# Optimization experiments

Hardware: AMD Instinct MI355X
Metric: run time of the kernel (lower is better)

## Reference

```python
import jax, jax.numpy as jnp
import numpy as np

B, N, D, H = 4, 2048, 256, 4
DH = D // H
SS = DH ** -0.25  # sqrt(scale), applied to both qk0 and qk1
EPS = 1e-5


def _split_heads(t):
    # [B, N, D] -> [B, H, N, DH]
    b, n, _ = t.shape
    return t.reshape(b, n, H, DH).transpose(0, 2, 1, 3)


def _merge_heads(t):
    # [B, H, N, DH] -> [B, N, D]
    b, h, n, dh = t.shape
    return t.transpose(0, 2, 1, 3).reshape(b, n, h * dh)


def _layernorm(x, g, b):
    mu = jnp.mean(x, axis=-1, keepdims=True)
    var = jnp.mean(jnp.square(x - mu), axis=-1, keepdims=True)
    return (x - mu) * jax.lax.rsqrt(var + EPS) * g + b


def setup_inputs() -> dict:
    key = jax.random.key(0)
    ks = jax.random.split(key, 16)
    s = 0.02
    return {
        "x0": jax.random.normal(ks[0], (B, N, D), jnp.float32),
        "x1": jax.random.normal(ks[1], (B, N, D), jnp.float32),
        # weights stored as [in, out] (y = x @ W + b), matching torch Linear math
        "Wqk": jax.random.normal(ks[2], (D, D), jnp.float32) * s,
        "bqk": jnp.zeros((D,), jnp.float32),
        "Wv": jax.random.normal(ks[3], (D, D), jnp.float32) * s,
        "bv": jnp.zeros((D,), jnp.float32),
        "Wo": jax.random.normal(ks[4], (D, D), jnp.float32) * s,
        "bo": jnp.zeros((D,), jnp.float32),
        "W1": jax.random.normal(ks[5], (2 * D, 2 * D), jnp.float32) * s,
        "b1": jnp.zeros((2 * D,), jnp.float32),
        "ln_g": jnp.ones((2 * D,), jnp.float32),
        "ln_b": jnp.zeros((2 * D,), jnp.float32),
        "W2": jax.random.normal(ks[6], (2 * D, D), jnp.float32) * s,
        "b2": jnp.zeros((D,), jnp.float32),
    }


def reference(x0, x1, Wqk, bqk, Wv, bv, Wo, bo, W1, b1, ln_g, ln_b, W2, b2):
    qk0 = _split_heads(x0 @ Wqk + bqk) * SS  # [B,H,N,DH]
    qk1 = _split_heads(x1 @ Wqk + bqk) * SS
    v0 = _split_heads(x0 @ Wv + bv)
    v1 = _split_heads(x1 @ Wv + bv)

    # single shared similarity matrix, reused for both softmax directions
    sim = jnp.einsum("bhid,bhjd->bhij", qk0, qk1)  # [B,H,N0,N1]
    attn01 = jax.nn.softmax(sim, axis=-1)                      # rows over j
    attn10 = jax.nn.softmax(jnp.swapaxes(sim, -1, -2), axis=-1)  # rows over i

    m0 = jnp.einsum("bhij,bhjd->bhid", attn01, v1)  # [B,H,N0,DH]
    m1 = jnp.einsum("bhji,bhjd->bhid", jnp.swapaxes(attn10, -1, -2), v0)

    m0 = _merge_heads(m0) @ Wo + bo  # [B,N,D]
    m1 = _merge_heads(m1) @ Wo + bo

    def ffn(x, m):
        h = jnp.concatenate([x, m], axis=-1) @ W1 + b1
        h = jax.nn.gelu(_layernorm(h, ln_g, ln_b), approximate=False)
        return x + h @ W2 + b2

    return ffn(x0, m0), ffn(x1, m1)
```

## Files before the change

### kernel.cpp

```cpp
#include <hip/hip_runtime.h>
#include <hip/hip_bf16.h>
#include <math.h>

#define DEV static __device__ __forceinline__

typedef float f32x4 __attribute__((ext_vector_type(4)));
typedef short s16x8 __attribute__((ext_vector_type(8)));
typedef unsigned short u16;
typedef unsigned int u32;

#define ROWS 16384
#define SSCALE 0.35355339059327379f

DEV f32x4 mfma16(s16x8 a, s16x8 b, f32x4 c) {
  return __builtin_amdgcn_mfma_f32_16x16x32_bf16(a, b, c, 0, 0, 0);
}

DEV float bf2f(u16 x) { u32 u = ((u32)x) << 16; float f; __builtin_memcpy(&f, &u, 4); return f; }
DEV u16 f2bf(float x) { __hip_bfloat16 b = __float2bfloat16(x); u16 r; __builtin_memcpy(&r, &b, 2); return r; }

DEV void gload_lds16(const void* g, void* l) {
  __builtin_amdgcn_global_load_lds((const __attribute__((address_space(1))) u32*)g,
                                   (__attribute__((address_space(3))) u32*)l, 16, 0, 0);
}

__global__ __launch_bounds__(256) void k_prep(
    const float* __restrict__ x0, const float* __restrict__ x1,
    const float* __restrict__ Wqk, const float* __restrict__ Wv,
    const float* __restrict__ Wo, const float* __restrict__ W1,
    const float* __restrict__ W2,
    u16* __restrict__ bt_qkv, u16* __restrict__ bt_o,
    u16* __restrict__ bt_1, u16* __restrict__ bt_2, u16* __restrict__ Xb)
{
  int tid = blockIdx.x * 256 + threadIdx.x;
  if (tid < 131072) {
    int c = tid >> 8, k = tid & 255;
    float v = (c < 256) ? Wqk[k * 256 + c] : Wv[k * 256 + (c - 256)];
    bt_qkv[tid] = f2bf(v);
  } else if (tid < 131072 + 65536) {
    int t = tid - 131072; int c = t >> 8, k = t & 255;
    bt_o[t] = f2bf(Wo[k * 256 + c]);
  } else if (tid < 131072 + 65536 + 262144) {
    int t = tid - (131072 + 65536); int c = t >> 9, k = t & 511;
    bt_1[t] = f2bf(W1[k * 512 + c]);
  } else if (tid < 589824) {
    int t = tid - (131072 + 65536 + 262144); int c = t >> 9, k = t & 511;
    bt_2[t] = f2bf(W2[k * 256 + c]);
  } else {
    int t = tid - 589824;
    float v = (t < 8192 * 256) ? x0[t] : x1[t - 8192 * 256];
    Xb[t] = f2bf(v);
  }
}

template <int KD, int K1, int EPI>
__global__ __launch_bounds__(256, 2) void k_gemm(
    const u16* __restrict__ A1, const u16* __restrict__ A2,
    const u16* __restrict__ Bt,
    const float* __restrict__ bias, const float* __restrict__ bias2,
    const float* __restrict__ res0, const float* __restrict__ res1,
    u16* __restrict__ outb, u16* __restrict__ outb2,
    float* __restrict__ outf, int Ncols)
{
  __shared__ char lds[32768];
  char* ldsA = lds;
  char* ldsB = lds + 16384;
  const int tid = threadIdx.x;
  const int lane = tid & 63;
  const int w = tid >> 6;
  const int wm = w >> 1, wn = w & 1;
  const int g = lane >> 4, li = lane & 15;
  const int m0 = blockIdx.x * 128, n0 = blockIdx.y * 128;

  auto stage = [&](int buf, int t) {
    const int k0 = t * 32;
#pragma unroll
    for (int it = 0; it < 2; ++it) {
      int chunk = it * 256 + w * 64 + lane;
      int row = chunk >> 2, c = chunk & 3;
      int kc = k0 + ((c ^ ((row >> 1) & 3)) << 3);
      const u16* src = (kc < K1) ? (A1 + (size_t)(m0 + row) * K1 + kc)
                                 : (A2 + (size_t)(m0 + row) * (KD - K1) + (kc - K1));
      gload_lds16(src, ldsA + buf * 8192 + (it * 256 + w * 64) * 16);
    }
#pragma unroll
    for (int it = 0; it < 2; ++it) {
      int chunk = it * 256 + w * 64 + lane;
      int row = chunk >> 2, c = chunk & 3;
      int kc = k0 + ((c ^ ((row >> 1) & 3)) << 3);
      gload_lds16(Bt + (size_t)(n0 + row) * KD + kc,
                  ldsB + buf * 8192 + (it * 256 + w * 64) * 16);
    }
  };

  f32x4 acc[4][4] = {};

  stage(0, 0);
  __syncthreads();
  const int NT = KD / 32;
  for (int t = 0; t < NT; ++t) {
    if (t + 1 < NT) stage((t + 1) & 1, t + 1);
    const char* bufA = ldsA + (t & 1) * 8192;
    const char* bufB = ldsB + (t & 1) * 8192;
    s16x8 af[4], bfr[4];
#pragma unroll
    for (int rt = 0; rt < 4; ++rt) {
      int row = wm * 64 + rt * 16 + li;
      af[rt] = *(const s16x8*)(bufA + row * 64 + ((g ^ ((row >> 1) & 3)) << 4));
    }
#pragma unroll
    for (int ct = 0; ct < 4; ++ct) {
      int col = wn * 64 + ct * 16 + li;
      bfr[ct] = *(const s16x8*)(bufB + col * 64 + ((g ^ ((col >> 1) & 3)) << 4));
    }
#pragma unroll
    for (int rt = 0; rt < 4; ++rt)
#pragma unroll
      for (int ct = 0; ct < 4; ++ct)
        acc[rt][ct] = mfma16(af[rt], bfr[ct], acc[rt][ct]);
    __syncthreads();
  }

#pragma unroll
  for (int rt = 0; rt < 4; ++rt) {
#pragma unroll
    for (int ct = 0; ct < 4; ++ct) {
#pragma unroll
      for (int r = 0; r < 4; ++r) {
        int grow = m0 + wm * 64 + rt * 16 + g * 4 + r;
        int gcol = n0 + wn * 64 + ct * 16 + li;
        float v = acc[rt][ct][r];
        if (EPI == 0) {
          int dir = grow >> 13, b = (grow >> 11) & 3, n = grow & 2047;
          if (gcol < 256) {
            int h = gcol >> 6, dh = gcol & 63;
            float q = (v + bias[gcol]) * SSCALE;
            outb[((size_t)(dir * 16 + b * 4 + h) * 2048 + n) * 64 + dh] = f2bf(q);
          } else {
            int c2 = gcol - 256; int h = c2 >> 6, dh = c2 & 63;
            outb2[((size_t)(dir * 16 + b * 4 + h) * 64 + dh) * 2048 + n] = f2bf(v + bias2[c2]);
          }
        } else if (EPI == 1) {
          outb[(size_t)grow * Ncols + gcol] = f2bf(v + bias[gcol]);
        } else {
          float x = (grow < 8192) ? res0[(size_t)grow * 256 + gcol]
                                  : res1[(size_t)(grow - 8192) * 256 + gcol];
          outf[(size_t)grow * 256 + gcol] = v + bias[gcol] + x;
        }
      }
    }
  }
}

__global__ __launch_bounds__(256, 2) void k_attn(
    const u16* __restrict__ qk, const u16* __restrict__ vt, u16* __restrict__ m_all)
{
  __shared__ char Kl[2][8192];
  __shared__ char Vl[2][8192];
  __shared__ char Pl[4][4096];
  const int tid = threadIdx.x, lane = tid & 63, w = tid >> 6;
  const int g = lane >> 4, li = lane & 15;
  const int qblk = blockIdx.x & 15;
  const int p = blockIdx.x >> 4;
  const int dir = p & 1;
  const int bh = p >> 1;
  const char* Qg = (const char*)qk + ((size_t)(dir * 16 + bh)) * 2048 * 64 * 2;
  const char* Kg = (const char*)qk + ((size_t)((dir ^ 1) * 16 + bh)) * 2048 * 64 * 2;
  const char* Vg = (const char*)vt + ((size_t)((dir ^ 1) * 16 + bh)) * 64 * 2048 * 2;
  const int q0 = qblk * 128 + w * 32;

  s16x8 qf[2][2];
#pragma unroll
  for (int qt = 0; qt < 2; ++qt)
#pragma unroll
    for (int ks = 0; ks < 2; ++ks)
      qf[qt][ks] = *(const s16x8*)(Qg + (size_t)(q0 + qt * 16 + li) * 128 + ks * 64 + g * 16);

  auto stageKV = [&](int buf, int jt) {
#pragma unroll
    for (int it = 0; it < 2; ++it) {
      int chunk = it * 256 + w * 64 + lane;
      int row = chunk >> 3, c = chunk & 7;
      int cc = (c ^ (row & 7)) << 4;
      gload_lds16(Kg + (size_t)(jt * 64 + row) * 128 + cc, &Kl[buf][(it * 256 + w * 64) * 16]);
    }
#pragma unroll
    for (int it = 0; it < 2; ++it) {
      int chunk = it * 256 + w * 64 + lane;
      int row = chunk >> 3, c = chunk & 7;
      int cc = (c ^ (row & 7)) << 4;
      gload_lds16(Vg + (size_t)row * 4096 + jt * 128 + cc, &Vl[buf][(it * 256 + w * 64) * 16]);
    }
  };

  f32x4 acco[2][4] = {};
  float accl[2][4] = {};

  stageKV(0, 0);
  __syncthreads();
  for (int jt = 0; jt < 32; ++jt) {
    if (jt + 1 < 32) stageKV((jt + 1) & 1, jt + 1);
    const char* Kb = Kl[jt & 1];
    const char* Vb = Vl[jt & 1];

    s16x8 vf[4][2];
#pragma unroll
    for (int dt = 0; dt < 4; ++dt)
#pragma unroll
      for (int ks = 0; ks < 2; ++ks) {
        int row = dt * 16 + li;
        vf[dt][ks] = *(const s16x8*)(Vb + row * 128 + (((ks * 4 + g) ^ (row & 7)) << 4));
      }

#pragma unroll
    for (int qt = 0; qt < 2; ++qt) {
#pragma unroll
      for (int kt = 0; kt < 4; ++kt) {
        f32x4 s = {0.f, 0.f, 0.f, 0.f};
#pragma unroll
        for (int ks = 0; ks < 2; ++ks) {
          int row = kt * 16 + li;
          s16x8 kf = *(const s16x8*)(Kb + row * 128 + (((ks * 4 + g) ^ (row & 7)) << 4));
          s = mfma16(qf[qt][ks], kf, s);
        }
#pragma unroll
        for (int r = 0; r < 4; ++r) {
          float pv = __expf(s[r]);
          accl[qt][r] += pv;
          int q = qt * 16 + g * 4 + r;
          int key = kt * 16 + li;
          *(u16*)(&Pl[w][q * 128 + ((key * 2) ^ ((q & 7) << 4))]) = f2bf(pv);
        }
      }
    }

#pragma unroll
    for (int qt = 0; qt < 2; ++qt) {
      s16x8 pf[2];
#pragma unroll
      for (int ks = 0; ks < 2; ++ks) {
        int qrow = qt * 16 + li;
        pf[ks] = *(const s16x8*)(&Pl[w][qrow * 128 + (((ks * 4 + g) << 4) ^ ((qrow & 7) << 4))]);
      }
#pragma unroll
      for (int dt = 0; dt < 4; ++dt)
#pragma unroll
        for (int ks = 0; ks < 2; ++ks)
          acco[qt][dt] = mfma16(pf[ks], vf[dt][ks], acco[qt][dt]);
    }
    __syncthreads();
  }

  float inv[2][4];
#pragma unroll
  for (int qt = 0; qt < 2; ++qt)
#pragma unroll
    for (int r = 0; r < 4; ++r) {
      float v = accl[qt][r];
      v += __shfl_xor(v, 1); v += __shfl_xor(v, 2);
      v += __shfl_xor(v, 4); v += __shfl_xor(v, 8);
      inv[qt][r] = 1.0f / v;
    }

  const int b = bh >> 2, h = bh & 3;
  const size_t rowbase = (size_t)dir * 8192 + (size_t)b * 2048 + q0;
#pragma unroll
  for (int qt = 0; qt < 2; ++qt)
#pragma unroll
    for (int dt = 0; dt < 4; ++dt)
#pragma unroll
      for (int r = 0; r < 4; ++r) {
        int q = qt * 16 + g * 4 + r;
        int dh = dt * 16 + li;
        m_all[(rowbase + q) * 256 + h * 64 + dh] = f2bf(acco[qt][dt][r] * inv[qt][r]);
      }
}

__global__ __launch_bounds__(256) void k_ln_gelu(
    const u16* __restrict__ h, const float* __restrict__ lg,
    const float* __restrict__ lb, u16* __restrict__ o)
{
  int lane = threadIdx.x & 63;
  size_t row = blockIdx.x * 4 + (threadIdx.x >> 6);
  s16x8 v = *(const s16x8*)(h + row * 512 + lane * 8);
  float f[8], s = 0.f, s2 = 0.f;
#pragma unroll
  for (int j = 0; j < 8; ++j) { f[j] = bf2f((u16)v[j]); s += f[j]; s2 += f[j] * f[j]; }
#pragma unroll
  for (int m = 1; m < 64; m <<= 1) { s += __shfl_xor(s, m); s2 += __shfl_xor(s2, m); }
  float mu = s * (1.0f / 512.0f);
  float var = s2 * (1.0f / 512.0f) - mu * mu;
  float rs = rsqrtf(var + 1e-5f);
  s16x8 ov;
#pragma unroll
  for (int j = 0; j < 8; ++j) {
    int c = lane * 8 + j;
    float y = (f[j] - mu) * rs * lg[c] + lb[c];
    float ge = 0.5f * y * (1.0f + erff(y * 0.70710678118654752f));
    ov[j] = (short)f2bf(ge);
  }
  *(s16x8*)(o + row * 512 + lane * 8) = ov;
}

extern "C" void kernel_launch(void* const* d_in, const int* in_sizes, int n_in,
                              void* d_out, int out_size, void* d_ws, size_t ws_size,
                              hipStream_t stream)
{
  const float* x0  = (const float*)d_in[0];
  const float* x1  = (const float*)d_in[1];
  const float* Wqk = (const float*)d_in[2];
  const float* bqk = (const float*)d_in[3];
  const float* Wv  = (const float*)d_in[4];
  const float* bv  = (const float*)d_in[5];
  const float* Wo  = (const float*)d_in[6];
  const float* bo  = (const float*)d_in[7];
  const float* W1  = (const float*)d_in[8];
  const float* b1  = (const float*)d_in[9];
  const float* lg  = (const float*)d_in[10];
  const float* lb  = (const float*)d_in[11];
  const float* W2  = (const float*)d_in[12];
  const float* b2  = (const float*)d_in[13];
  float* out = (float*)d_out;
  char* ws = (char*)d_ws;

  u16* Xb    = (u16*)(ws + 0);
  u16* qk    = (u16*)(ws + 8388608);
  u16* vt    = (u16*)(ws + 16777216);
  u16* m_all = (u16*)(ws + 25165824);
  u16* mo    = (u16*)(ws + 33554432);
  u16* hpre  = (u16*)(ws + 41943040);
  u16* gact  = (u16*)(ws + 58720256);
  u16* btqkv = (u16*)(ws + 75497472);
  u16* bto   = (u16*)(ws + 75759616);
  u16* bt1   = (u16*)(ws + 75890688);
  u16* bt2   = (u16*)(ws + 76414976);

  k_prep<<<dim3(18688), dim3(256), 0, stream>>>(x0, x1, Wqk, Wv, Wo, W1, W2,
                                                btqkv, bto, bt1, bt2, Xb);
  k_gemm<256, 256, 0><<<dim3(128, 4), dim3(256), 0, stream>>>(
      Xb, nullptr, btqkv, bqk, bv, nullptr, nullptr, qk, vt, nullptr, 512);
  k_attn<<<dim3(512), dim3(256), 0, stream>>>(qk, vt, m_all);
  k_gemm<256, 256, 1><<<dim3(128, 2), dim3(256), 0, stream>>>(
      m_all, nullptr, bto, bo, nullptr, nullptr, nullptr, mo, nullptr, nullptr, 256);
  k_gemm<512, 256, 1><<<dim3(128, 4), dim3(256), 0, stream>>>(
      Xb, mo, bt1, b1, nullptr, nullptr, nullptr, hpre, nullptr, nullptr, 512);
  k_ln_gelu<<<dim3(4096), dim3(256), 0, stream>>>(hpre, lg, lb, gact);
  k_gemm<512, 512, 3><<<dim3(128, 2), dim3(256), 0, stream>>>(
      gact, nullptr, bt2, b2, nullptr, x0, x1, nullptr, nullptr, out, 256);
}
```

Before: 257.3 us.

## Split attention keys across two blocks, add combine kernel, narrow GEMM tiles

Attention now splits the key range in half, so twice as many blocks run. Each block writes unnormalized fp32 partial outputs and row sums, and a new combine kernel adds them and normalizes to bf16. The S tile is computed transposed (K as the A operand), so P can be written to LDS as packed 8-byte stores and the row sums need fewer shuffles. The Wo and W2 GEMMs get a BN=64 tile variant to double their grid, and the V-transpose epilogue uses packed 4-wide stores. This adds an extra launch and fp32 partial traffic in exchange for better occupancy on the 256-CU part.

```diff
diff --git a/kernel.cpp b/kernel.cpp
--- a/kernel.cpp
+++ b/kernel.cpp
@@ -8,6 +8,8 @@
 typedef short s16x8 __attribute__((ext_vector_type(8)));
 typedef unsigned short u16;
 typedef unsigned int u32;
+typedef u32 u32x2 __attribute__((ext_vector_type(2)));
+typedef u16 u16x4 __attribute__((ext_vector_type(4)));
 
 #define ROWS 16384
 #define SSCALE 0.35355339059327379f
@@ -53,7 +55,7 @@
   }
 }
 
-template <int KD, int K1, int EPI>
+template <int KD, int K1, int EPI, int BN>
 __global__ __launch_bounds__(256, 2) void k_gemm(
     const u16* __restrict__ A1, const u16* __restrict__ A2,
     const u16* __restrict__ Bt,
@@ -62,15 +64,17 @@
     u16* __restrict__ outb, u16* __restrict__ outb2,
     float* __restrict__ outf, int Ncols)
 {
-  __shared__ char lds[32768];
+  constexpr int MR = (BN == 128) ? 4 : 2;
+  __shared__ char lds[16384 + 2 * BN * 64];
   char* ldsA = lds;
   char* ldsB = lds + 16384;
   const int tid = threadIdx.x;
   const int lane = tid & 63;
   const int w = tid >> 6;
-  const int wm = w >> 1, wn = w & 1;
+  const int wm = (BN == 128) ? (w >> 1) : w;
+  const int wn = (BN == 128) ? (w & 1) : 0;
   const int g = lane >> 4, li = lane & 15;
-  const int m0 = blockIdx.x * 128, n0 = blockIdx.y * 128;
+  const int m0 = blockIdx.x * 128, n0 = blockIdx.y * BN;
 
   auto stage = [&](int buf, int t) {
     const int k0 = t * 32;
@@ -84,16 +88,16 @@
       gload_lds16(src, ldsA + buf * 8192 + (it * 256 + w * 64) * 16);
     }
 #pragma unroll
-    for (int it = 0; it < 2; ++it) {
+    for (int it = 0; it < BN / 64; ++it) {
       int chunk = it * 256 + w * 64 + lane;
       int row = chunk >> 2, c = chunk & 3;
       int kc = k0 + ((c ^ ((row >> 1) & 3)) << 3);
       gload_lds16(Bt + (size_t)(n0 + row) * KD + kc,
-                  ldsB + buf * 8192 + (it * 256 + w * 64) * 16);
+                  ldsB + buf * (BN * 64) + (it * 256 + w * 64) * 16);
     }
   };
 
-  f32x4 acc[4][4] = {};
+  f32x4 acc[MR][4] = {};
 
   stage(0, 0);
   __syncthreads();
@@ -101,11 +105,11 @@
   for (int t = 0; t < NT; ++t) {
     if (t + 1 < NT) stage((t + 1) & 1, t + 1);
     const char* bufA = ldsA + (t & 1) * 8192;
-    const char* bufB = ldsB + (t & 1) * 8192;
-    s16x8 af[4], bfr[4];
-#pragma unroll
-    for (int rt = 0; rt < 4; ++rt) {
-      int row = wm * 64 + rt * 16 + li;
+    const char* bufB = ldsB + (t & 1) * (BN * 64);
+    s16x8 af[MR], bfr[4];
+#pragma unroll
+    for (int rt = 0; rt < MR; ++rt) {
+      int row = wm * (MR * 16) + rt * 16 + li;
       af[rt] = *(const s16x8*)(bufA + row * 64 + ((g ^ ((row >> 1) & 3)) << 4));
     }
 #pragma unroll
@@ -114,7 +118,7 @@
       bfr[ct] = *(const s16x8*)(bufB + col * 64 + ((g ^ ((col >> 1) & 3)) << 4));
     }
 #pragma unroll
-    for (int rt = 0; rt < 4; ++rt)
+    for (int rt = 0; rt < MR; ++rt)
 #pragma unroll
       for (int ct = 0; ct < 4; ++ct)
         acc[rt][ct] = mfma16(af[rt], bfr[ct], acc[rt][ct]);
@@ -122,38 +126,47 @@
   }
 
 #pragma unroll
-  for (int rt = 0; rt < 4; ++rt) {
+  for (int rt = 0; rt < MR; ++rt) {
 #pragma unroll
     for (int ct = 0; ct < 4; ++ct) {
-#pragma unroll
-      for (int r = 0; r < 4; ++r) {
-        int grow = m0 + wm * 64 + rt * 16 + g * 4 + r;
-        int gcol = n0 + wn * 64 + ct * 16 + li;
-        float v = acc[rt][ct][r];
-        if (EPI == 0) {
-          int dir = grow >> 13, b = (grow >> 11) & 3, n = grow & 2047;
-          if (gcol < 256) {
-            int h = gcol >> 6, dh = gcol & 63;
-            float q = (v + bias[gcol]) * SSCALE;
-            outb[((size_t)(dir * 16 + b * 4 + h) * 2048 + n) * 64 + dh] = f2bf(q);
-          } else {
-            int c2 = gcol - 256; int h = c2 >> 6, dh = c2 & 63;
-            outb2[((size_t)(dir * 16 + b * 4 + h) * 64 + dh) * 2048 + n] = f2bf(v + bias2[c2]);
+      const int growb = m0 + wm * (MR * 16) + rt * 16 + g * 4;
+      const int gcol = n0 + wn * 64 + ct * 16 + li;
+      if (EPI == 0) {
+        const int dir = growb >> 13, b = (growb >> 11) & 3, n = growb & 2047;
+        if (gcol < 256) {
+          const int h = gcol >> 6, dh = gcol & 63;
+#pragma unroll
+          for (int r = 0; r < 4; ++r) {
+            float q = (acc[rt][ct][r] + bias[gcol]) * SSCALE;
+            outb[((size_t)(dir * 16 + b * 4 + h) * 2048 + (n + r)) * 64 + dh] = f2bf(q);
           }
-        } else if (EPI == 1) {
-          outb[(size_t)grow * Ncols + gcol] = f2bf(v + bias[gcol]);
         } else {
+          const int c2 = gcol - 256, h = c2 >> 6, dh = c2 & 63;
+          u16x4 pk;
+#pragma unroll
+          for (int r = 0; r < 4; ++r) pk[r] = f2bf(acc[rt][ct][r] + bias2[c2]);
+          *(u16x4*)(outb2 + ((size_t)(dir * 16 + b * 4 + h) * 64 + dh) * 2048 + n) = pk;
+        }
+      } else if (EPI == 1) {
+#pragma unroll
+        for (int r = 0; r < 4; ++r)
+          outb[(size_t)(growb + r) * Ncols + gcol] = f2bf(acc[rt][ct][r] + bias[gcol]);
+      } else {
+#pragma unroll
+        for (int r = 0; r < 4; ++r) {
+          int grow = growb + r;
           float x = (grow < 8192) ? res0[(size_t)grow * 256 + gcol]
                                   : res1[(size_t)(grow - 8192) * 256 + gcol];
-          outf[(size_t)grow * 256 + gcol] = v + bias[gcol] + x;
+          outf[(size_t)grow * 256 + gcol] = acc[rt][ct][r] + bias[gcol] + x;
         }
       }
     }
   }
 }
 
-__global__ __launch_bounds__(256, 2) void k_attn(
-    const u16* __restrict__ qk, const u16* __restrict__ vt, u16* __restrict__ m_all)
+__global__ __launch_bounds__(256, 3) void k_attn(
+    const u16* __restrict__ qk, const u16* __restrict__ vt,
+    float* __restrict__ Opart, float* __restrict__ lpart)
 {
   __shared__ char Kl[2][8192];
   __shared__ char Vl[2][8192];
@@ -161,12 +174,14 @@
   const int tid = threadIdx.x, lane = tid & 63, w = tid >> 6;
   const int g = lane >> 4, li = lane & 15;
   const int qblk = blockIdx.x & 15;
-  const int p = blockIdx.x >> 4;
+  const int half = (blockIdx.x >> 4) & 1;
+  const int p = blockIdx.x >> 5;
   const int dir = p & 1;
   const int bh = p >> 1;
-  const char* Qg = (const char*)qk + ((size_t)(dir * 16 + bh)) * 2048 * 64 * 2;
-  const char* Kg = (const char*)qk + ((size_t)((dir ^ 1) * 16 + bh)) * 2048 * 64 * 2;
-  const char* Vg = (const char*)vt + ((size_t)((dir ^ 1) * 16 + bh)) * 64 * 2048 * 2;
+  const int pidx = dir * 16 + bh;
+  const char* Qg = (const char*)qk + (size_t)pidx * 2048 * 128;
+  const char* Kg = (const char*)qk + (size_t)((dir ^ 1) * 16 + bh) * 2048 * 128;
+  const char* Vg = (const char*)vt + (size_t)((dir ^ 1) * 16 + bh) * 2048 * 128;
   const int q0 = qblk * 128 + w * 32;
 
   s16x8 qf[2][2];
@@ -177,103 +192,117 @@
       qf[qt][ks] = *(const s16x8*)(Qg + (size_t)(q0 + qt * 16 + li) * 128 + ks * 64 + g * 16);
 
   auto stageKV = [&](int buf, int jt) {
+    const size_t krow0 = (size_t)(half * 1024 + jt * 64);
 #pragma unroll
     for (int it = 0; it < 2; ++it) {
       int chunk = it * 256 + w * 64 + lane;
       int row = chunk >> 3, c = chunk & 7;
       int cc = (c ^ (row & 7)) << 4;
-      gload_lds16(Kg + (size_t)(jt * 64 + row) * 128 + cc, &Kl[buf][(it * 256 + w * 64) * 16]);
+      gload_lds16(Kg + (krow0 + row) * 128 + cc, &Kl[buf][(it * 256 + w * 64) * 16]);
     }
 #pragma unroll
     for (int it = 0; it < 2; ++it) {
       int chunk = it * 256 + w * 64 + lane;
       int row = chunk >> 3, c = chunk & 7;
       int cc = (c ^ (row & 7)) << 4;
-      gload_lds16(Vg + (size_t)row * 4096 + jt * 128 + cc, &Vl[buf][(it * 256 + w * 64) * 16]);
+      gload_lds16(Vg + (size_t)row * 4096 + half * 2048 + jt * 128 + cc,
+                  &Vl[buf][(it * 256 + w * 64) * 16]);
     }
   };
 
   f32x4 acco[2][4] = {};
-  float accl[2][4] = {};
+  float accl[2] = {0.f, 0.f};
 
   stageKV(0, 0);
   __syncthreads();
-  for (int jt = 0; jt < 32; ++jt) {
-    if (jt + 1 < 32) stageKV((jt + 1) & 1, jt + 1);
+  for (int jt = 0; jt < 16; ++jt) {
+    if (jt + 1 < 16) stageKV((jt + 1) & 1, jt + 1);
     const char* Kb = Kl[jt & 1];
     const char* Vb = Vl[jt & 1];
 
-    s16x8 vf[4][2];
-#pragma unroll
-    for (int dt = 0; dt < 4; ++dt)
-#pragma unroll
-      for (int ks = 0; ks < 2; ++ks) {
-        int row = dt * 16 + li;
-        vf[dt][ks] = *(const s16x8*)(Vb + row * 128 + (((ks * 4 + g) ^ (row & 7)) << 4));
+#pragma unroll
+    for (int kt = 0; kt < 4; ++kt) {
+      const int krow = kt * 16 + li;
+      s16x8 kf0 = *(const s16x8*)(Kb + krow * 128 + ((g ^ (krow & 7)) << 4));
+      s16x8 kf1 = *(const s16x8*)(Kb + krow * 128 + (((4 + g) ^ (krow & 7)) << 4));
+#pragma unroll
+      for (int qt = 0; qt < 2; ++qt) {
+        f32x4 s = {0.f, 0.f, 0.f, 0.f};
+        s = mfma16(kf0, qf[qt][0], s);
+        s = mfma16(kf1, qf[qt][1], s);
+        float p0 = __expf(s[0]), p1 = __expf(s[1]);
+        float p2 = __expf(s[2]), p3 = __expf(s[3]);
+        accl[qt] += (p0 + p1) + (p2 + p3);
+        u32x2 pk;
+        pk.x = (u32)f2bf(p0) | ((u32)f2bf(p1) << 16);
+        pk.y = (u32)f2bf(p2) | ((u32)f2bf(p3) << 16);
+        int addr = ((qt * 16 + li) * 128 + kt * 32 + g * 8) ^ ((li & 7) << 4);
+        *(u32x2*)(&Pl[w][addr]) = pk;
       }
-
-#pragma unroll
-    for (int qt = 0; qt < 2; ++qt) {
-#pragma unroll
-      for (int kt = 0; kt < 4; ++kt) {
-        f32x4 s = {0.f, 0.f, 0.f, 0.f};
-#pragma unroll
-        for (int ks = 0; ks < 2; ++ks) {
-          int row = kt * 16 + li;
-          s16x8 kf = *(const s16x8*)(Kb + row * 128 + (((ks * 4 + g) ^ (row & 7)) << 4));
-          s = mfma16(qf[qt][ks], kf, s);
-        }
-#pragma unroll
-        for (int r = 0; r < 4; ++r) {
-          float pv = __expf(s[r]);
-          accl[qt][r] += pv;
-          int q = qt * 16 + g * 4 + r;
-          int key = kt * 16 + li;
-          *(u16*)(&Pl[w][q * 128 + ((key * 2) ^ ((q & 7) << 4))]) = f2bf(pv);
-        }
+    }
+
+#pragma unroll
+    for (int ks = 0; ks < 2; ++ks) {
+      s16x8 vfr[4];
+#pragma unroll
+      for (int dt = 0; dt < 4; ++dt) {
+        const int vrow = dt * 16 + li;
+        vfr[dt] = *(const s16x8*)(Vb + vrow * 128 + (((ks * 4 + g) ^ (vrow & 7)) << 4));
       }
-    }
-
-#pragma unroll
-    for (int qt = 0; qt < 2; ++qt) {
-      s16x8 pf[2];
-#pragma unroll
-      for (int ks = 0; ks < 2; ++ks) {
-        int qrow = qt * 16 + li;
-        pf[ks] = *(const s16x8*)(&Pl[w][qrow * 128 + (((ks * 4 + g) << 4) ^ ((qrow & 7) << 4))]);
+#pragma unroll
+      for (int qt = 0; qt < 2; ++qt) {
+        s16x8 pf = *(const s16x8*)(
+            &Pl[w][((qt * 16 + li) * 128 + ks * 64 + g * 16) ^ ((li & 7) << 4)]);
+#pragma unroll
+        for (int dt = 0; dt < 4; ++dt)
+          acco[qt][dt] = mfma16(pf, vfr[dt], acco[qt][dt]);
       }
-#pragma unroll
-      for (int dt = 0; dt < 4; ++dt)
-#pragma unroll
-        for (int ks = 0; ks < 2; ++ks)
-          acco[qt][dt] = mfma16(pf[ks], vf[dt][ks], acco[qt][dt]);
     }
     __syncthreads();
   }
 
-  float inv[2][4];
-#pragma unroll
-  for (int qt = 0; qt < 2; ++qt)
-#pragma unroll
-    for (int r = 0; r < 4; ++r) {
-      float v = accl[qt][r];
-      v += __shfl_xor(v, 1); v += __shfl_xor(v, 2);
-      v += __shfl_xor(v, 4); v += __shfl_xor(v, 8);
-      inv[qt][r] = 1.0f / v;
-    }
+#pragma unroll
+  for (int qt = 0; qt < 2; ++qt) {
+    float v = accl[qt];
+    v += __shfl_xor(v, 16);
+    v += __shfl_xor(v, 32);
+    accl[qt] = v;
+  }
 
   const int b = bh >> 2, h = bh & 3;
   const size_t rowbase = (size_t)dir * 8192 + (size_t)b * 2048 + q0;
+  float* Oh = Opart + (size_t)half * 4194304;
 #pragma unroll
   for (int qt = 0; qt < 2; ++qt)
 #pragma unroll
     for (int dt = 0; dt < 4; ++dt)
 #pragma unroll
-      for (int r = 0; r < 4; ++r) {
-        int q = qt * 16 + g * 4 + r;
-        int dh = dt * 16 + li;
-        m_all[(rowbase + q) * 256 + h * 64 + dh] = f2bf(acco[qt][dt][r] * inv[qt][r]);
-      }
+      for (int r = 0; r < 4; ++r)
+        Oh[(rowbase + qt * 16 + g * 4 + r) * 256 + h * 64 + dt * 16 + li] = acco[qt][dt][r];
+  if (lane < 16) {
+#pragma unroll
+    for (int qt = 0; qt < 2; ++qt)
+      lpart[half * 65536 + pidx * 2048 + q0 + qt * 16 + li] = accl[qt];
+  }
+}
+
+__global__ __launch_bounds__(256) void k_combine(
+    const float* __restrict__ Op, const float* __restrict__ lp,
+    u16* __restrict__ m_all)
+{
+  int t = blockIdx.x * 256 + threadIdx.x;
+  int row = t >> 6, quad = t & 63;
+  int dh0 = quad * 4;
+  int dir = row >> 13, b = (row >> 11) & 3, n = row & 2047, h = dh0 >> 6;
+  int pidx = dir * 16 + b * 4 + h;
+  float l = lp[pidx * 2048 + n] + lp[65536 + pidx * 2048 + n];
+  float invl = 1.0f / l;
+  f32x4 o0 = *(const f32x4*)(Op + (size_t)row * 256 + dh0);
+  f32x4 o1 = *(const f32x4*)(Op + 4194304 + (size_t)row * 256 + dh0);
+  u16x4 r4;
+#pragma unroll
+  for (int j = 0; j < 4; ++j) r4[j] = f2bf((o0[j] + o1[j]) * invl);
+  *(u16x4*)(m_all + (size_t)row * 256 + dh0) = r4;
 }
 
 __global__ __launch_bounds__(256) void k_ln_gelu(
@@ -323,28 +352,31 @@
   float* out = (float*)d_out;
   char* ws = (char*)d_ws;
 
-  u16* Xb    = (u16*)(ws + 0);
-  u16* qk    = (u16*)(ws + 8388608);
-  u16* vt    = (u16*)(ws + 16777216);
-  u16* m_all = (u16*)(ws + 25165824);
-  u16* mo    = (u16*)(ws + 33554432);
-  u16* hpre  = (u16*)(ws + 41943040);
-  u16* gact  = (u16*)(ws + 58720256);
-  u16* btqkv = (u16*)(ws + 75497472);
-  u16* bto   = (u16*)(ws + 75759616);
-  u16* bt1   = (u16*)(ws + 75890688);
-  u16* bt2   = (u16*)(ws + 76414976);
+  u16*   Xb    = (u16*)(ws + 0);
+  u16*   qk    = (u16*)(ws + 8388608);
+  u16*   vt    = (u16*)(ws + 16777216);
+  u16*   m_all = (u16*)(ws + 25165824);
+  float* lpart = (float*)(ws + 33554432);
+  u16*   mo    = (u16*)(ws + 34078720);
+  float* Opart = (float*)(ws + 42467328);
+  u16*   hpre  = (u16*)(ws + 42467328);
+  u16*   gact  = (u16*)(ws + 59244544);
+  u16*   btqkv = (u16*)(ws + 76021760);
+  u16*   bto   = (u16*)(ws + 76283904);
+  u16*   bt1   = (u16*)(ws + 76414976);
+  u16*   bt2   = (u16*)(ws + 76939264);
 
   k_prep<<<dim3(18688), dim3(256), 0, stream>>>(x0, x1, Wqk, Wv, Wo, W1, W2,
                                                 btqkv, bto, bt1, bt2, Xb);
-  k_gemm<256, 256, 0><<<dim3(128, 4), dim3(256), 0, stream>>>(
+  k_gemm<256, 256, 0, 128><<<dim3(128, 4), dim3(256), 0, stream>>>(
       Xb, nullptr, btqkv, bqk, bv, nullptr, nullptr, qk, vt, nullptr, 512);
-  k_attn<<<dim3(512), dim3(256), 0, stream>>>(qk, vt, m_all);
-  k_gemm<256, 256, 1><<<dim3(128, 2), dim3(256), 0, stream>>>(
+  k_attn<<<dim3(1024), dim3(256), 0, stream>>>(qk, vt, Opart, lpart);
+  k_combine<<<dim3(4096), dim3(256), 0, stream>>>(Opart, lpart, m_all);
+  k_gemm<256, 256, 1, 64><<<dim3(128, 4), dim3(256), 0, stream>>>(
       m_all, nullptr, bto, bo, nullptr, nullptr, nullptr, mo, nullptr, nullptr, 256);
-  k_gemm<512, 256, 1><<<dim3(128, 4), dim3(256), 0, stream>>>(
+  k_gemm<512, 256, 1, 128><<<dim3(128, 4), dim3(256), 0, stream>>>(
       Xb, mo, bt1, b1, nullptr, nullptr, nullptr, hpre, nullptr, nullptr, 512);
   k_ln_gelu<<<dim3(4096), dim3(256), 0, stream>>>(hpre, lg, lb, gact);
-  k_gemm<512, 512, 3><<<dim3(128, 2), dim3(256), 0, stream>>>(
+  k_gemm<512, 512, 3, 64><<<dim3(128, 4), dim3(256), 0, stream>>>(
       gact, nullptr, bt2, b2, nullptr, x0, x1, nullptr, nullptr, out, 256);
 }
```

After: 235.7 us. -8.4%, faster.
